# Performance work log

Measured on AMD Instinct MI355X. Metric: run time of the kernel, lower is better.

## Reference

```python
import jax, jax.numpy as jnp
import numpy as np

B, T, C, H = 8, 2048, 1024, 16
S = C // H
LN_EPS = 1e-5


def setup_inputs() -> dict:
    key = jax.random.key(0)
    ks = jax.random.split(key, 12)
    w = lambda k: jax.random.normal(k, (C, C), dtype=jnp.float32) * 0.02
    return {
        "x": jax.random.normal(ks[0], (B, T, C), dtype=jnp.float32),
        "time_mix_k": jax.random.uniform(ks[1], (1, 1, C), dtype=jnp.float32),
        "time_mix_v": jax.random.uniform(ks[2], (1, 1, C), dtype=jnp.float32),
        "time_mix_r": jax.random.uniform(ks[3], (1, 1, C), dtype=jnp.float32),
        # keep exp(time_decay) < 1 for numerical stability over T=2048 steps
        "time_decay": -jax.random.uniform(ks[4], (H, S), minval=0.1, maxval=5.0, dtype=jnp.float32),
        "time_first": jax.random.uniform(ks[5], (H, S), dtype=jnp.float32),
        "Wk": w(ks[6]), "Wv": w(ks[7]), "Wr": w(ks[8]), "Wo": w(ks[9]),
        "ln_g": jnp.ones((C,), jnp.float32),
        "ln_b": jnp.zeros((C,), jnp.float32),
    }


def reference(x, time_mix_k, time_mix_v, time_mix_r, time_decay, time_first, Wk, Wv, Wr, Wo, ln_g, ln_b):
    Bx, Tx, Cx = x.shape
    # time_shift: xx[t] = x[t-1], xx[0] = 0
    xx = jnp.pad(x, ((0, 0), (1, 0), (0, 0)))[:, :-1]
    xk = x * time_mix_k + xx * (1 - time_mix_k)
    xv = x * time_mix_v + xx * (1 - time_mix_v)
    xr = x * time_mix_r + xx * (1 - time_mix_r)
    proj = lambda z, W: jnp.einsum('btc,dc->btd', z, W).reshape(Bx, Tx, H, S)
    k = proj(xk, Wk)  # [B,T,H,S]
    v = proj(xv, Wv)
    r = proj(xr, Wr)
    kv = k * v  # elementwise per-channel 'at' (diagonal of outer-product state)
    decay = jnp.exp(time_decay)  # [H,S]

    def step(state, inp):
        kv_t, r_t = inp  # [B,H,S] each
        state = kv_t + decay * state
        o = r_t * (time_first * kv_t + state)
        return state, o

    kvT = jnp.swapaxes(kv, 0, 1)  # [T,B,H,S]
    rT = jnp.swapaxes(r, 0, 1)
    _, outT = jax.lax.scan(step, jnp.zeros((Bx, H, S), x.dtype), (kvT, rT))
    out = jnp.swapaxes(outT, 0, 1).reshape(Bx, Tx, Cx)
    mu = out.mean(-1, keepdims=True)
    var = out.var(-1, keepdims=True)
    out = (out - mu) / jnp.sqrt(var + LN_EPS) * ln_g + ln_b
    return jnp.einsum('btc,dc->btd', out, Wo)
```

## Files before the change

kernel.cpp:

```cpp
#include <hip/hip_runtime.h>

#define Bsz 8
#define Tn  2048
#define Cn  1024
#define Hn  16
#define Sn  64
#define Mn  (Bsz * Tn)
#define NC  32
#define LCH (Tn / NC)
#define Kd  1024
#define NKT (Kd / 64)

typedef __attribute__((ext_vector_type(8))) short bf16x8;
typedef __attribute__((ext_vector_type(4))) float f32x4;

__device__ __forceinline__ unsigned short f2bf(float f) {
  union { float f; unsigned int u; } v;
  v.f = f;
  unsigned int r = (v.u + 0x7FFFu + ((v.u >> 16) & 1u)) >> 16;
  return (unsigned short)r;
}
__device__ __forceinline__ float bf2f(unsigned short u) {
  union { unsigned int u; float f; } v;
  v.u = ((unsigned int)u) << 16;
  return v.f;
}

__global__ void wconv_kernel(const float* __restrict__ Wk, const float* __restrict__ Wv,
                             const float* __restrict__ Wr, const float* __restrict__ Wo,
                             unsigned short* __restrict__ out) {
  int i = blockIdx.x * blockDim.x + threadIdx.x;
  int which = i >> 18;
  int off = (i & 0x3FFFF) * 4;
  const float* src = which == 0 ? Wk : which == 1 ? Wv : which == 2 ? Wr : Wo;
  float4 f = *(const float4*)(src + off);
  ushort4 o;
  o.x = f2bf(f.x); o.y = f2bf(f.y); o.z = f2bf(f.z); o.w = f2bf(f.w);
  *(ushort4*)(out + (size_t)which * (Cn * Cn) + off) = o;
}

__global__ void mix3_kernel(const float* __restrict__ x,
                            const float* __restrict__ tmk, const float* __restrict__ tmv,
                            const float* __restrict__ tmr,
                            unsigned short* __restrict__ ok, unsigned short* __restrict__ ov,
                            unsigned short* __restrict__ orr) {
  int idx = blockIdx.x * blockDim.x + threadIdx.x;
  int c4 = idx & (Cn / 4 - 1);
  int bt = idx >> 8;
  int t = bt & (Tn - 1);
  size_t base = (size_t)bt * Cn + c4 * 4;
  float4 xv = *(const float4*)(x + base);
  float4 xxv = {0.f, 0.f, 0.f, 0.f};
  if (t != 0) xxv = *(const float4*)(x + base - Cn);
  float4 dx = {xv.x - xxv.x, xv.y - xxv.y, xv.z - xxv.z, xv.w - xxv.w};
  float4 tk = *(const float4*)(tmk + c4 * 4);
  float4 tv = *(const float4*)(tmv + c4 * 4);
  float4 tr = *(const float4*)(tmr + c4 * 4);
  ushort4 a, b, c;
  a.x = f2bf(xxv.x + tk.x * dx.x); a.y = f2bf(xxv.y + tk.y * dx.y);
  a.z = f2bf(xxv.z + tk.z * dx.z); a.w = f2bf(xxv.w + tk.w * dx.w);
  b.x = f2bf(xxv.x + tv.x * dx.x); b.y = f2bf(xxv.y + tv.y * dx.y);
  b.z = f2bf(xxv.z + tv.z * dx.z); b.w = f2bf(xxv.w + tv.w * dx.w);
  c.x = f2bf(xxv.x + tr.x * dx.x); c.y = f2bf(xxv.y + tr.y * dx.y);
  c.z = f2bf(xxv.z + tr.z * dx.z); c.w = f2bf(xxv.w + tr.w * dx.w);
  *(ushort4*)(ok + base) = a;
  *(ushort4*)(ov + base) = b;
  *(ushort4*)(orr + base) = c;
}

__device__ __forceinline__ void gload_lds16(const void* g, void* l) {
  __builtin_amdgcn_global_load_lds((const __attribute__((address_space(1))) void*)g,
                                   (__attribute__((address_space(3))) void*)l, 16, 0, 0);
}

#define PHASE(H, KS, LOADB, PRE)                                                   \
  {                                                                                \
    _Pragma("unroll") for (int mi4 = 0; mi4 < 4; ++mi4) {                          \
      const int row = wm * 128 + (H) * 64 + mi4 * 16 + l15;                        \
      aF[mi4] = *(const bf16x8*)(ldsc + dbase + row * 128 +                        \
                                 ((((KS) * 4 + lg) ^ (row & 7)) << 4));            \
    }                                                                              \
    if (LOADB) {                                                                   \
      _Pragma("unroll") for (int nj = 0; nj < 4; ++nj) {                           \
        const int row = wn * 64 + nj * 16 + l15;                                   \
        bF[nj] = *(const bf16x8*)(ldsc + dbase + 32768 + row * 128 +               \
                                  ((((KS) * 4 + lg) ^ (row & 7)) << 4));           \
      }                                                                            \
    }                                                                              \
    PRE;                                                                           \
    __builtin_amdgcn_s_barrier();                                                  \
    asm volatile("s_waitcnt lgkmcnt(0)" ::: "memory");                             \
    __builtin_amdgcn_sched_barrier(0);                                             \
    __builtin_amdgcn_s_setprio(1);                                                 \
    _Pragma("unroll") for (int mi4 = 0; mi4 < 4; ++mi4)                            \
      _Pragma("unroll") for (int nj = 0; nj < 4; ++nj)                             \
        acc[(H) * 4 + mi4][nj] = __builtin_amdgcn_mfma_f32_16x16x32_bf16(          \
            aF[mi4], bF[nj], acc[(H) * 4 + mi4][nj], 0, 0, 0);                     \
    __builtin_amdgcn_s_setprio(0);                                                 \
    __builtin_amdgcn_s_barrier();                                                  \
  }

template <bool OUTBF16>
__global__ __launch_bounds__(512, 2) void gemm8p(const unsigned short* __restrict__ A,
                                                 const unsigned short* __restrict__ Bt,
                                                 void* __restrict__ Cm) {
  __shared__ unsigned short lds[65536];
  char* ldsc = (char*)lds;
  const int tid = threadIdx.x;
  const int wid = tid >> 6, lane = tid & 63;
  const int wm = wid >> 2, wn = wid & 3;
  const int l15 = lane & 15, lg = lane >> 4;
  int bid = ((int)blockIdx.x & 7) * 32 + ((int)blockIdx.x >> 3);
  const int mt = bid >> 2, nt = bid & 3;
  const int m0 = mt * 256, n0 = nt * 256;

  const unsigned short* Ag = A + (size_t)m0 * Kd;
  const unsigned short* Bg = Bt + (size_t)n0 * Kd;

  auto stageU = [&](const unsigned short* gbase, int ktt, int rbase, int Loff) {
#pragma unroll
    for (int j = 0; j < 2; ++j) {
      const int il = j * 512 + tid;
      const int r = rbase + (il >> 3);
      const int c = (il & 7) ^ (r & 7);
      gload_lds16(gbase + (size_t)r * Kd + ktt * 64 + c * 8,
                  ldsc + Loff + rbase * 128 + il * 16);
    }
  };
  auto stageKT = [&](int ktt, int base) {
    stageU(Ag, ktt, 0, base);
    stageU(Ag, ktt, 128, base);
    stageU(Bg, ktt, 0, base + 32768);
    stageU(Bg, ktt, 128, base + 32768);
  };

  f32x4 acc[8][4] = {};
  bf16x8 aF[4], bF[4];

  stageKT(0, 0);
  asm volatile("s_waitcnt vmcnt(0)" ::: "memory");
  __builtin_amdgcn_s_barrier();

  for (int kt = 0; kt < NKT; ++kt) {
    const int dbase = (kt & 1) << 16;
    const int nd = dbase ^ 65536;
    PHASE(0, 0, 1, if (kt + 1 < NKT) stageKT(kt + 1, nd))
    PHASE(1, 0, 0, ;)
    PHASE(1, 1, 1, ;)
    PHASE(0, 1, 0, asm volatile("s_waitcnt vmcnt(0)" ::: "memory"))
  }

  if (OUTBF16) {
    char* tb = ldsc + wid * 16384;
#pragma unroll
    for (int mi = 0; mi < 8; ++mi)
#pragma unroll
      for (int nj = 0; nj < 4; ++nj)
#pragma unroll
        for (int rr = 0; rr < 4; ++rr) {
          const int row = mi * 16 + lg * 4 + rr;
          const int col = nj * 16 + l15;
          *(unsigned short*)(tb + row * 128 + ((col * 2) ^ ((row & 7) << 4))) =
              f2bf(acc[mi][nj][rr]);
        }
    asm volatile("s_waitcnt lgkmcnt(0)" ::: "memory");
    __builtin_amdgcn_sched_barrier(0);
    const int orl = lane >> 3, och = lane & 7;
#pragma unroll
    for (int it = 0; it < 16; ++it) {
      const int row = it * 8 + orl;
      uint4 vv = *(const uint4*)(tb + row * 128 + ((och * 16) ^ ((row & 7) << 4)));
      const int gr = m0 + wm * 128 + row;
      const int gc = n0 + wn * 64 + och * 8;
      *(uint4*)((unsigned short*)Cm + (size_t)gr * Cn + gc) = vv;
    }
  } else {
#pragma unroll
    for (int mi = 0; mi < 8; ++mi)
#pragma unroll
      for (int nj = 0; nj < 4; ++nj)
#pragma unroll
        for (int rr = 0; rr < 4; ++rr) {
          const int row = m0 + wm * 128 + mi * 16 + lg * 4 + rr;
          const int col = n0 + wn * 64 + nj * 16 + l15;
          ((float*)Cm)[(size_t)row * Cn + col] = acc[mi][nj][rr];
        }
  }
}

__global__ void scan_phase1(const unsigned short* __restrict__ k,
                            const unsigned short* __restrict__ v,
                            const float* __restrict__ td, float* __restrict__ cs) {
  int blk = blockIdx.x;
  int c = blk & (NC - 1);
  int bh = blk >> 5;
  int b = bh >> 4;
  int h = bh & 15;
  int s = threadIdx.x;
  float decay = expf(td[h * Sn + s]);
  size_t base = ((size_t)(b * Tn + c * LCH)) * Cn + h * Sn + s;
  float st = 0.f;
#pragma unroll 8
  for (int i = 0; i < LCH; ++i) {
    float kv = bf2f(k[base]) * bf2f(v[base]);
    st = kv + decay * st;
    base += Cn;
  }
  cs[(size_t)blk * Sn + s] = st;
}

__global__ void scan_phase2(const float* __restrict__ td, float* __restrict__ cs) {
  int bh = blockIdx.x;
  int h = bh & 15;
  int s = threadIdx.x;
  float dL = expf(td[h * Sn + s] * (float)LCH);
  float carry = 0.f;
  for (int c = 0; c < NC; ++c) {
    size_t idx = ((size_t)bh * NC + c) * Sn + s;
    float sc = cs[idx];
    cs[idx] = carry;
    carry = sc + dL * carry;
  }
}

__global__ void scan_phase3(const unsigned short* __restrict__ k,
                            const unsigned short* __restrict__ v,
                            const unsigned short* __restrict__ r,
                            const float* __restrict__ td, const float* __restrict__ tf,
                            const float* __restrict__ cs,
                            unsigned short* __restrict__ out) {
  int blk = blockIdx.x;
  int c = blk & (NC - 1);
  int bh = blk >> 5;
  int b = bh >> 4;
  int h = bh & 15;
  int s = threadIdx.x;
  float decay = expf(td[h * Sn + s]);
  float first = tf[h * Sn + s];
  float st = cs[(size_t)blk * Sn + s];
  size_t base = ((size_t)(b * Tn + c * LCH)) * Cn + h * Sn + s;
#pragma unroll 8
  for (int i = 0; i < LCH; ++i) {
    float kv = bf2f(k[base]) * bf2f(v[base]);
    st = kv + decay * st;
    out[base] = f2bf(bf2f(r[base]) * (first * kv + st));
    base += Cn;
  }
}

__global__ __launch_bounds__(256) void ln_kernel(const unsigned short* __restrict__ in,
                                                 const float* __restrict__ g,
                                                 const float* __restrict__ bb,
                                                 unsigned short* __restrict__ out) {
  int row = blockIdx.x;
  int tid = threadIdx.x;
  size_t base = (size_t)row * Cn + tid * 4;
  ushort4 uv = *(const ushort4*)(in + base);
  float4 xv = {bf2f(uv.x), bf2f(uv.y), bf2f(uv.z), bf2f(uv.w)};
  float sum = xv.x + xv.y + xv.z + xv.w;
  float ss = xv.x * xv.x + xv.y * xv.y + xv.z * xv.z + xv.w * xv.w;
#pragma unroll
  for (int off = 32; off >= 1; off >>= 1) {
    sum += __shfl_down(sum, off, 64);
    ss += __shfl_down(ss, off, 64);
  }
  __shared__ float s1[4], s2[4];
  if ((tid & 63) == 0) { s1[tid >> 6] = sum; s2[tid >> 6] = ss; }
  __syncthreads();
  sum = s1[0] + s1[1] + s1[2] + s1[3];
  ss = s2[0] + s2[1] + s2[2] + s2[3];
  float mu = sum * (1.f / Cn);
  float var = ss * (1.f / Cn) - mu * mu;
  float rstd = rsqrtf(var + 1e-5f);
  float4 gv = *(const float4*)(g + tid * 4);
  float4 bv = *(const float4*)(bb + tid * 4);
  ushort4 o;
  o.x = f2bf((xv.x - mu) * rstd * gv.x + bv.x);
  o.y = f2bf((xv.y - mu) * rstd * gv.y + bv.y);
  o.z = f2bf((xv.z - mu) * rstd * gv.z + bv.z);
  o.w = f2bf((xv.w - mu) * rstd * gv.w + bv.w);
  *(ushort4*)(out + base) = o;
}

extern "C" void kernel_launch(void* const* d_in, const int* in_sizes, int n_in,
                              void* d_out, int out_size, void* d_ws, size_t ws_size,
                              hipStream_t stream) {
  const float* x   = (const float*)d_in[0];
  const float* tmk = (const float*)d_in[1];
  const float* tmv = (const float*)d_in[2];
  const float* tmr = (const float*)d_in[3];
  const float* td  = (const float*)d_in[4];
  const float* tf  = (const float*)d_in[5];
  const float* Wk  = (const float*)d_in[6];
  const float* Wv  = (const float*)d_in[7];
  const float* Wr  = (const float*)d_in[8];
  const float* Wo  = (const float*)d_in[9];
  const float* lng = (const float*)d_in[10];
  const float* lnb = (const float*)d_in[11];
  float* out = (float*)d_out;

  char* ws = (char*)d_ws;
  const size_t MB = 1024 * 1024;
  unsigned short* wbf  = (unsigned short*)(ws);
  unsigned short* xk   = (unsigned short*)(ws + 8 * MB);
  unsigned short* xv_  = (unsigned short*)(ws + 40 * MB);
  unsigned short* xr   = (unsigned short*)(ws + 72 * MB);
  unsigned short* bufK = (unsigned short*)(ws + 104 * MB);
  unsigned short* bufV = (unsigned short*)(ws + 136 * MB);
  unsigned short* bufR = (unsigned short*)(ws + 168 * MB);
  unsigned short* preLN = xk;
  unsigned short* lnout = xv_;
  float* chunkS = (float*)(ws + 200 * MB);

  const int gemm_grid = (Mn / 256) * (Cn / 256);
  const int mix_grid = Mn * (Cn / 4) / 256;

  wconv_kernel<<<4 * Cn * Cn / 4 / 256, 256, 0, stream>>>(Wk, Wv, Wr, Wo, wbf);
  mix3_kernel<<<mix_grid, 256, 0, stream>>>(x, tmk, tmv, tmr, xk, xv_, xr);

  gemm8p<true><<<gemm_grid, 512, 0, stream>>>(xk,  wbf + 0 * (size_t)Cn * Cn, bufK);
  gemm8p<true><<<gemm_grid, 512, 0, stream>>>(xv_, wbf + 1 * (size_t)Cn * Cn, bufV);
  gemm8p<true><<<gemm_grid, 512, 0, stream>>>(xr,  wbf + 2 * (size_t)Cn * Cn, bufR);

  scan_phase1<<<Bsz * Hn * NC, 64, 0, stream>>>(bufK, bufV, td, chunkS);
  scan_phase2<<<Bsz * Hn, 64, 0, stream>>>(td, chunkS);
  scan_phase3<<<Bsz * Hn * NC, 64, 0, stream>>>(bufK, bufV, bufR, td, tf, chunkS, preLN);

  ln_kernel<<<Mn, 256, 0, stream>>>(preLN, lng, lnb, lnout);

  gemm8p<false><<<gemm_grid, 512, 0, stream>>>(lnout, wbf + 3 * (size_t)Cn * Cn, out);

  (void)in_sizes; (void)n_in; (void)out_size; (void)ws_size;
}
```

Before: 255.1 us.

## Reorder GEMM tile staging so the A upper half lands before its compute phase

Restructures the bf16 GEMM's global-to-LDS prefetch. Each wave now stages 8-row slices, with B loaded first and the A bands ordered so the half-0 rows (bands 0 and 2) arrive before the half-1 rows. The prefetch issue moves from phase 0 to phase 1, and the waits become partial (vmcnt(2)) so the first phase of the next tile can start before the last A slices finish. The aim is finer overlap of memory latency with MFMA work. The trade-off is a more fragile wait-count scheme that depends on load ordering, and a prefetch issued later in the iteration.

```diff
diff --git a/kernel.cpp b/kernel.cpp
--- a/kernel.cpp
+++ b/kernel.cpp
@@ -73,7 +73,7 @@
                                    (__attribute__((address_space(3))) void*)l, 16, 0, 0);
 }
 
-#define PHASE(H, KS, LOADB, PRE)                                                   \
+#define PHASE(H, KS, LOADB, PRE, POST)                                             \
   {                                                                                \
     _Pragma("unroll") for (int mi4 = 0; mi4 < 4; ++mi4) {                          \
       const int row = wm * 128 + (H) * 64 + mi4 * 16 + l15;                        \
@@ -97,6 +97,7 @@
         acc[(H) * 4 + mi4][nj] = __builtin_amdgcn_mfma_f32_16x16x32_bf16(          \
             aF[mi4], bF[nj], acc[(H) * 4 + mi4][nj], 0, 0, 0);                     \
     __builtin_amdgcn_s_setprio(0);                                                 \
+    POST;                                                                          \
     __builtin_amdgcn_s_barrier();                                                  \
   }
 
@@ -117,37 +118,38 @@
   const unsigned short* Ag = A + (size_t)m0 * Kd;
   const unsigned short* Bg = Bt + (size_t)n0 * Kd;
 
-  auto stageU = [&](const unsigned short* gbase, int ktt, int rbase, int Loff) {
-#pragma unroll
-    for (int j = 0; j < 2; ++j) {
-      const int il = j * 512 + tid;
-      const int r = rbase + (il >> 3);
-      const int c = (il & 7) ^ (r & 7);
-      gload_lds16(gbase + (size_t)r * Kd + ktt * 64 + c * 8,
-                  ldsc + Loff + rbase * 128 + il * 16);
-    }
+  auto stageSlice = [&](const unsigned short* gbase, int ktt, int band, int Loff) {
+    const int r = band * 64 + wid * 8 + (lane >> 3);
+    const int c = (lane & 7) ^ (r & 7);
+    gload_lds16(gbase + (size_t)r * Kd + ktt * 64 + c * 8,
+                ldsc + Loff + (band * 64 + wid * 8) * 128 + lane * 16);
   };
-  auto stageKT = [&](int ktt, int base) {
-    stageU(Ag, ktt, 0, base);
-    stageU(Ag, ktt, 128, base);
-    stageU(Bg, ktt, 0, base + 32768);
-    stageU(Bg, ktt, 128, base + 32768);
+  auto stage8 = [&](int ktt, int base) {
+    stageSlice(Bg, ktt, 0, base + 32768);
+    stageSlice(Bg, ktt, 1, base + 32768);
+    stageSlice(Bg, ktt, 2, base + 32768);
+    stageSlice(Bg, ktt, 3, base + 32768);
+    stageSlice(Ag, ktt, 0, base);
+    stageSlice(Ag, ktt, 2, base);
+    stageSlice(Ag, ktt, 1, base);
+    stageSlice(Ag, ktt, 3, base);
   };
 
   f32x4 acc[8][4] = {};
   bf16x8 aF[4], bF[4];
 
-  stageKT(0, 0);
-  asm volatile("s_waitcnt vmcnt(0)" ::: "memory");
+  stage8(0, 0);
+  asm volatile("s_waitcnt vmcnt(2)" ::: "memory");
   __builtin_amdgcn_s_barrier();
 
   for (int kt = 0; kt < NKT; ++kt) {
     const int dbase = (kt & 1) << 16;
     const int nd = dbase ^ 65536;
-    PHASE(0, 0, 1, if (kt + 1 < NKT) stageKT(kt + 1, nd))
-    PHASE(1, 0, 0, ;)
-    PHASE(1, 1, 1, ;)
-    PHASE(0, 1, 0, asm volatile("s_waitcnt vmcnt(0)" ::: "memory"))
+    const bool st = (kt + 1 < NKT);
+    PHASE(0, 0, 1, ;, asm volatile("s_waitcnt vmcnt(0)" ::: "memory"))
+    PHASE(1, 0, 0, if (st) stage8(kt + 1, nd), ;)
+    PHASE(1, 1, 1, ;, ;)
+    PHASE(0, 1, 0, ;, asm volatile("s_waitcnt vmcnt(2)" ::: "memory"))
   }
 
   if (OUTBF16) {
```

After: 257.5 us. No clear change (+0.9%).
